# Optimization experiments

Hardware: AMD Instinct MI355X
Metric: run time of the kernel (lower is better)

## Reference

```python
import jax, jax.numpy as jnp
import numpy as np

LR = 0.01  # constraint relaxation learning rate (module default)
EPS = 1e-6


def setup_inputs() -> dict:
    key = jax.random.key(0)
    k1, k2, k3, k4 = jax.random.split(key, 4)
    N, E, K = 8192, 262144, 65536
    positions = jax.random.normal(k1, (N, 3), dtype=jnp.float32)
    edge_index = jax.random.randint(k2, (2, E), 0, N, dtype=jnp.int32)
    dist_idx = jax.random.randint(k3, (K, 2), 0, N, dtype=jnp.int32)
    dist_target = jax.random.uniform(k4, (K,), dtype=jnp.float32) * 2.0
    min_dist = jnp.ones((1,), dtype=jnp.float32) * 0.5
    return {"positions": positions, "edge_index": edge_index,
            "dist_idx": dist_idx, "dist_target": dist_target,
            "min_dist": min_dist}


def reference(positions, edge_index, dist_idx, dist_target, min_dist):
    x = positions  # (N, 3)
    N = x.shape[0]

    # --- distance constraints: ||x_i - x_j|| -> d_ij (Jacobi-style update) ---
    i, j = dist_idx[:, 0], dist_idx[:, 1]
    vec = x[i] - x[j]                                  # (K, 3)
    dist = jnp.sqrt(jnp.sum(vec * vec, axis=-1) + 1e-12)
    valid = (dist > EPS) & (i != j)
    coef = jnp.where(valid, LR * 0.5 * (dist - dist_target) / dist, 0.0)
    corr = coef[:, None] * vec                         # (K, 3)
    x = x.at[i].add(-corr).at[j].add(corr)

    # --- collision constraints: push apart all pairs with dist < min_dist ---
    md = min_dist[0]
    sq = jnp.sum(x * x, axis=-1)                       # (N,)
    d2 = jnp.maximum(sq[:, None] + sq[None, :] - 2.0 * (x @ x.T), 1e-12)
    dmat = jnp.sqrt(d2)                                # (N, N) pairwise distances
    mask = (dmat < md) & (dmat > EPS)                  # excludes diagonal (dist ~ 0)
    w = jnp.where(mask, (md - dmat) / dmat, 0.0) * (0.5 * LR)  # (N, N)
    # correction_i = sum_j w_ij * (x_i - x_j)
    x = x + x * jnp.sum(w, axis=-1, keepdims=True) - w @ x

    # --- gaussian curvature via normalized graph Laplacian ---
    e = jnp.clip(edge_index, 0, N - 1)
    adj = jnp.zeros((N, N), dtype=x.dtype).at[e[0], e[1]].set(1.0)
    adj = adj + adj.T
    deg = adj.sum(axis=1)
    dinv = jnp.where(deg == 0, 0.0, jnp.power(deg + EPS, -0.5))
    # L_norm @ x = x - D^{-1/2} A D^{-1/2} x (diagonal scaling, same math)
    lap = x - dinv[:, None] * (adj @ (dinv[:, None] * x))
    curvature = jnp.sqrt(jnp.sum(lap * lap, axis=-1) + 1e-12)  # (N,)

    return x, curvature
```

## Files before the change

### kernel.cpp

```cpp
#include <hip/hip_runtime.h>
#include <math.h>

#define N_NODES 8192
#define WPR 256
#define LR_C 0.01f
#define EPS_C 1e-6f
#define NJ 32

__global__ __launch_bounds__(256) void init_clear(const float4* __restrict__ pos4,
                                                  float4* __restrict__ x1_4,
                                                  uint4* __restrict__ adj,
                                                  uint4* __restrict__ deg4) {
    int gid = blockIdx.x * blockDim.x + threadIdx.x;
    adj[gid] = make_uint4(0u, 0u, 0u, 0u);
    if (gid < 6144) x1_4[gid] = pos4[gid];
    if (gid < 2048) deg4[gid] = make_uint4(0u, 0u, 0u, 0u);
}

__global__ __launch_bounds__(256) void scatter_adj(
        const float* __restrict__ x0, const int* __restrict__ dist_idx,
        const float* __restrict__ dist_target, const int* __restrict__ edge_index,
        float* __restrict__ x1, unsigned int* __restrict__ A,
        unsigned int* __restrict__ B, int* __restrict__ deg,
        int K, int E, int nbK) {
    int blk = blockIdx.x;
    if (blk < nbK) {
        int k = blk * 256 + threadIdx.x;
        if (k >= K) return;
        int i = dist_idx[2 * k], j = dist_idx[2 * k + 1];
        float ax = x0[3 * i], ay = x0[3 * i + 1], az = x0[3 * i + 2];
        float bx = x0[3 * j], by = x0[3 * j + 1], bz = x0[3 * j + 2];
        float vx = ax - bx, vy = ay - by, vz = az - bz;
        float dist = sqrtf(vx * vx + vy * vy + vz * vz + 1e-12f);
        bool valid = (dist > EPS_C) && (i != j);
        float coef = valid ? (LR_C * 0.5f) * (dist - dist_target[k]) / dist : 0.0f;
        if (coef != 0.0f) {
            float cx = coef * vx, cy = coef * vy, cz = coef * vz;
            atomicAdd(&x1[3 * i],     -cx);
            atomicAdd(&x1[3 * i + 1], -cy);
            atomicAdd(&x1[3 * i + 2], -cz);
            atomicAdd(&x1[3 * j],      cx);
            atomicAdd(&x1[3 * j + 1],  cy);
            atomicAdd(&x1[3 * j + 2],  cz);
        }
    } else {
        int k = (blk - nbK) * 256 + threadIdx.x;
        if (k >= E) return;
        int a = edge_index[k];
        int b = edge_index[E + k];
        a = min(max(a, 0), N_NODES - 1);
        b = min(max(b, 0), N_NODES - 1);
        unsigned int bitb = 1u << (b & 31);
        unsigned int bita = 1u << (a & 31);
        unsigned int old = atomicOr(&A[a * WPR + (b >> 5)], bitb);
        if (!(old & bitb)) atomicAdd(&deg[a], 1);
        old = atomicOr(&B[b * WPR + (a >> 5)], bita);
        if (!(old & bita)) atomicAdd(&deg[b], 1);
    }
}

__global__ __launch_bounds__(256) void repulsion_partial(
        const float* __restrict__ x1, const float* __restrict__ min_dist,
        float4* __restrict__ partials) {
    __shared__ float4 pj[256];
    int t = threadIdx.x;
    int jbase = blockIdx.y * 256;
    int i = blockIdx.x * 256 + t;
    {
        int j = jbase + t;
        float a = x1[3 * j], b = x1[3 * j + 1], c = x1[3 * j + 2];
        pj[t] = make_float4(a, b, c, a * a + b * b + c * c);
    }
    __syncthreads();
    float xi = x1[3 * i], yi = x1[3 * i + 1], zi = x1[3 * i + 2];
    float sqi = xi * xi + yi * yi + zi * zi;
    float md = min_dist[0];
    const float c0 = 0.5f * LR_C;
    float c1 = c0 * md;
    float S = 0.f, axc = 0.f, ayc = 0.f, azc = 0.f;
    if (blockIdx.x == blockIdx.y) {
        int di = t;
        #pragma unroll 4
        for (int jj = 0; jj < 256; ++jj) {
            float4 p = pj[jj];
            float dot = fmaf(xi, p.x, fmaf(yi, p.y, zi * p.z));
            float d2 = fmaf(-2.0f, dot, sqi + p.w);
            float r = __builtin_amdgcn_rsqf(fmaxf(d2, 1e-12f));
            float w = fmaxf(fmaf(c1, r, -c0), 0.0f);
            w = (d2 > 1e-12f && jj != di) ? w : 0.0f;
            S += w;
            axc = fmaf(w, p.x, axc);
            ayc = fmaf(w, p.y, ayc);
            azc = fmaf(w, p.z, azc);
        }
    } else {
        #pragma unroll 4
        for (int jj = 0; jj < 256; ++jj) {
            float4 p = pj[jj];
            float dot = fmaf(xi, p.x, fmaf(yi, p.y, zi * p.z));
            float d2 = fmaf(-2.0f, dot, sqi + p.w);
            float r = __builtin_amdgcn_rsqf(fmaxf(d2, 1e-12f));
            float w = fmaxf(fmaf(c1, r, -c0), 0.0f);
            w = (d2 > 1e-12f) ? w : 0.0f;
            S += w;
            axc = fmaf(w, p.x, axc);
            ayc = fmaf(w, p.y, ayc);
            azc = fmaf(w, p.z, azc);
        }
    }
    partials[blockIdx.y * N_NODES + i] = make_float4(axc, ayc, azc, S);
}

__global__ __launch_bounds__(256) void finalize(
        const float* __restrict__ x1, const float4* __restrict__ partials,
        const int* __restrict__ deg,
        float* __restrict__ x2, float* __restrict__ out_x,
        float* __restrict__ dinv, float4* __restrict__ z4) {
    int i = blockIdx.x * blockDim.x + threadIdx.x;
    if (i >= N_NODES) return;
    float S = 0.f, axc = 0.f, ayc = 0.f, azc = 0.f;
    #pragma unroll
    for (int c = 0; c < NJ; ++c) {
        float4 p = partials[c * N_NODES + i];
        axc += p.x; ayc += p.y; azc += p.z; S += p.w;
    }
    float xi = x1[3 * i], yi = x1[3 * i + 1], zi = x1[3 * i + 2];
    float ox = xi + xi * S - axc;
    float oy = yi + yi * S - ayc;
    float oz = zi + zi * S - azc;
    x2[3 * i] = ox; x2[3 * i + 1] = oy; x2[3 * i + 2] = oz;
    out_x[3 * i] = ox; out_x[3 * i + 1] = oy; out_x[3 * i + 2] = oz;
    int d = deg[i];
    float dv = (d == 0) ? 0.0f : 1.0f / sqrtf((float)d + EPS_C);
    dinv[i] = dv;
    z4[i] = make_float4(dv * ox, dv * oy, dv * oz, dv);
}

__global__ __launch_bounds__(256) void lap_kernel(
        const unsigned int* __restrict__ A, const unsigned int* __restrict__ B,
        const float* __restrict__ x2, const float* __restrict__ dinv,
        const float4* __restrict__ z4, float* __restrict__ out_curv) {
    int row = (blockIdx.x * blockDim.x + threadIdx.x) >> 6;
    int lane = threadIdx.x & 63;
    if (row >= N_NODES) return;
    float axc = 0.f, ayc = 0.f, azc = 0.f;
    #pragma unroll
    for (int q = 0; q < 4; ++q) {
        int wi = q * 64 + lane;
        unsigned int w = A[(size_t)row * WPR + wi];
        while (w) {
            int b = __ffs(w) - 1; w &= w - 1;
            float4 z = z4[wi * 32 + b];
            axc += z.x; ayc += z.y; azc += z.z;
        }
        w = B[(size_t)row * WPR + wi];
        while (w) {
            int b = __ffs(w) - 1; w &= w - 1;
            float4 z = z4[wi * 32 + b];
            axc += z.x; ayc += z.y; azc += z.z;
        }
    }
    for (int off = 32; off; off >>= 1) {
        axc += __shfl_down(axc, off);
        ayc += __shfl_down(ayc, off);
        azc += __shfl_down(azc, off);
    }
    if (lane == 0) {
        float dv = dinv[row];
        float lx = x2[3 * row]     - dv * axc;
        float ly = x2[3 * row + 1] - dv * ayc;
        float lz = x2[3 * row + 2] - dv * azc;
        out_curv[row] = sqrtf(lx * lx + ly * ly + lz * lz + 1e-12f);
    }
}

extern "C" void kernel_launch(void* const* d_in, const int* in_sizes, int n_in,
                              void* d_out, int out_size, void* d_ws, size_t ws_size,
                              hipStream_t stream) {
    const float* positions   = (const float*)d_in[0];
    const int*   edge_index  = (const int*)d_in[1];
    const int*   dist_idx    = (const int*)d_in[2];
    const float* dist_target = (const float*)d_in[3];
    const float* min_dist    = (const float*)d_in[4];
    float* out = (float*)d_out;

    const int E = in_sizes[1] / 2;
    const int K = in_sizes[2] / 2;

    char* ws = (char*)d_ws;
    const size_t X1_OFF   = 0;
    const size_t X2_OFF   = X1_OFF + (size_t)N_NODES * 3 * 4;
    const size_t Z4_OFF   = X2_OFF + (size_t)N_NODES * 3 * 4;
    const size_t DINV_OFF = Z4_OFF + (size_t)N_NODES * 16;
    const size_t DEG_OFF  = DINV_OFF + (size_t)N_NODES * 4;
    const size_t PART_OFF = DEG_OFF + (size_t)N_NODES * 4;
    const size_t ADJ_OFF  = PART_OFF + (size_t)NJ * N_NODES * 16;
    const size_t ADJ_BYTES = (size_t)N_NODES * WPR * 4;

    float* x1         = (float*)(ws + X1_OFF);
    float* x2         = (float*)(ws + X2_OFF);
    float4* z4        = (float4*)(ws + Z4_OFF);
    float* dinv       = (float*)(ws + DINV_OFF);
    int*   deg        = (int*)(ws + DEG_OFF);
    float4* partials  = (float4*)(ws + PART_OFF);
    unsigned int* A   = (unsigned int*)(ws + ADJ_OFF);
    unsigned int* B   = (unsigned int*)(ws + ADJ_OFF + ADJ_BYTES);

    init_clear<<<4096, 256, 0, stream>>>((const float4*)positions,
                                         (float4*)x1, (uint4*)A, (uint4*)deg);

    int nbK = (K + 255) / 256;
    int nbE = (E + 255) / 256;
    scatter_adj<<<nbK + nbE, 256, 0, stream>>>(
        positions, dist_idx, dist_target, edge_index, x1, A, B, deg, K, E, nbK);

    dim3 grid_rep(N_NODES / 256, NJ);
    repulsion_partial<<<grid_rep, 256, 0, stream>>>(x1, min_dist, partials);

    finalize<<<N_NODES / 256, 256, 0, stream>>>(x1, partials, deg,
                                                x2, out, dinv, z4);

    lap_kernel<<<N_NODES / 4, 256, 0, stream>>>(A, B, x2, dinv, z4,
                                                out + 3 * N_NODES);
}
```

Measured before the change: 118.5 us.

## Replace dense adjacency bitmaps with hashed edge dedup and atomic Laplacian scatter

Drops the two dense N×N adjacency bitmaps, which cost 16 MB to clear and a full row scan in the Laplacian kernel. Edges are now deduplicated with an open-addressing hash on (a,b) keys via atomicCAS, and each edge gets a uniqueness flag. The Laplacian becomes a per-edge atomic scatter of z4 into an accumulator, followed by a small curvature kernel. In exchange it adds hash probing contention, float atomics (nondeterministic summation order) and one extra kernel launch.

```diff
diff --git a/kernel.cpp b/kernel.cpp
--- a/kernel.cpp
+++ b/kernel.cpp
@@ -2,26 +2,43 @@
 #include <math.h>
 
 #define N_NODES 8192
-#define WPR 256
 #define LR_C 0.01f
 #define EPS_C 1e-6f
 #define NJ 32
+#define HASH_SLOTS (1u << 20)
+#define HEMPTY 0xFFFFFFFFu
+
+#define HASH_V 262144
+#define X1_V   6144
+#define LACC_V 6144
+#define DEG_V  2048
+#define TOT_V  (HASH_V + X1_V + LACC_V + DEG_V)
 
 __global__ __launch_bounds__(256) void init_clear(const float4* __restrict__ pos4,
                                                   float4* __restrict__ x1_4,
-                                                  uint4* __restrict__ adj,
+                                                  uint4* __restrict__ hash4,
+                                                  float4* __restrict__ lacc4,
                                                   uint4* __restrict__ deg4) {
     int gid = blockIdx.x * blockDim.x + threadIdx.x;
-    adj[gid] = make_uint4(0u, 0u, 0u, 0u);
-    if (gid < 6144) x1_4[gid] = pos4[gid];
-    if (gid < 2048) deg4[gid] = make_uint4(0u, 0u, 0u, 0u);
-}
-
-__global__ __launch_bounds__(256) void scatter_adj(
+    if (gid < HASH_V) {
+        hash4[gid] = make_uint4(HEMPTY, HEMPTY, HEMPTY, HEMPTY);
+    } else if (gid < HASH_V + X1_V) {
+        int t = gid - HASH_V;
+        x1_4[t] = pos4[t];
+    } else if (gid < HASH_V + X1_V + LACC_V) {
+        int t = gid - (HASH_V + X1_V);
+        lacc4[t] = make_float4(0.f, 0.f, 0.f, 0.f);
+    } else if (gid < TOT_V) {
+        int t = gid - (HASH_V + X1_V + LACC_V);
+        deg4[t] = make_uint4(0u, 0u, 0u, 0u);
+    }
+}
+
+__global__ __launch_bounds__(256) void scatter_hash(
         const float* __restrict__ x0, const int* __restrict__ dist_idx,
         const float* __restrict__ dist_target, const int* __restrict__ edge_index,
-        float* __restrict__ x1, unsigned int* __restrict__ A,
-        unsigned int* __restrict__ B, int* __restrict__ deg,
+        float* __restrict__ x1, unsigned int* __restrict__ hash,
+        unsigned char* __restrict__ flags, int* __restrict__ deg,
         int K, int E, int nbK) {
     int blk = blockIdx.x;
     if (blk < nbK) {
@@ -50,12 +67,20 @@
         int b = edge_index[E + k];
         a = min(max(a, 0), N_NODES - 1);
         b = min(max(b, 0), N_NODES - 1);
-        unsigned int bitb = 1u << (b & 31);
-        unsigned int bita = 1u << (a & 31);
-        unsigned int old = atomicOr(&A[a * WPR + (b >> 5)], bitb);
-        if (!(old & bitb)) atomicAdd(&deg[a], 1);
-        old = atomicOr(&B[b * WPR + (a >> 5)], bita);
-        if (!(old & bita)) atomicAdd(&deg[b], 1);
+        unsigned int key = ((unsigned)a << 13) | (unsigned)b;
+        unsigned int h = (key * 2654435761u) >> 12;
+        bool unique = false;
+        while (true) {
+            unsigned int old = atomicCAS(&hash[h], HEMPTY, key);
+            if (old == HEMPTY) { unique = true; break; }
+            if (old == key)   { break; }
+            h = (h + 1) & (HASH_SLOTS - 1);
+        }
+        flags[k] = unique ? 1 : 0;
+        if (unique) {
+            atomicAdd(&deg[a], 1);
+            atomicAdd(&deg[b], 1);
+        }
     }
 }
 
@@ -136,42 +161,36 @@
     z4[i] = make_float4(dv * ox, dv * oy, dv * oz, dv);
 }
 
-__global__ __launch_bounds__(256) void lap_kernel(
-        const unsigned int* __restrict__ A, const unsigned int* __restrict__ B,
+__global__ __launch_bounds__(256) void lap_scatter(
+        const int* __restrict__ edge_index, const unsigned char* __restrict__ flags,
+        const float4* __restrict__ z4, float* __restrict__ lacc, int E) {
+    int k = blockIdx.x * blockDim.x + threadIdx.x;
+    if (k >= E) return;
+    if (!flags[k]) return;
+    int a = edge_index[k];
+    int b = edge_index[E + k];
+    a = min(max(a, 0), N_NODES - 1);
+    b = min(max(b, 0), N_NODES - 1);
+    float4 zb = z4[b];
+    float4 za = z4[a];
+    atomicAdd(&lacc[3 * a],     zb.x);
+    atomicAdd(&lacc[3 * a + 1], zb.y);
+    atomicAdd(&lacc[3 * a + 2], zb.z);
+    atomicAdd(&lacc[3 * b],     za.x);
+    atomicAdd(&lacc[3 * b + 1], za.y);
+    atomicAdd(&lacc[3 * b + 2], za.z);
+}
+
+__global__ __launch_bounds__(256) void curvature(
         const float* __restrict__ x2, const float* __restrict__ dinv,
-        const float4* __restrict__ z4, float* __restrict__ out_curv) {
-    int row = (blockIdx.x * blockDim.x + threadIdx.x) >> 6;
-    int lane = threadIdx.x & 63;
-    if (row >= N_NODES) return;
-    float axc = 0.f, ayc = 0.f, azc = 0.f;
-    #pragma unroll
-    for (int q = 0; q < 4; ++q) {
-        int wi = q * 64 + lane;
-        unsigned int w = A[(size_t)row * WPR + wi];
-        while (w) {
-            int b = __ffs(w) - 1; w &= w - 1;
-            float4 z = z4[wi * 32 + b];
-            axc += z.x; ayc += z.y; azc += z.z;
-        }
-        w = B[(size_t)row * WPR + wi];
-        while (w) {
-            int b = __ffs(w) - 1; w &= w - 1;
-            float4 z = z4[wi * 32 + b];
-            axc += z.x; ayc += z.y; azc += z.z;
-        }
-    }
-    for (int off = 32; off; off >>= 1) {
-        axc += __shfl_down(axc, off);
-        ayc += __shfl_down(ayc, off);
-        azc += __shfl_down(azc, off);
-    }
-    if (lane == 0) {
-        float dv = dinv[row];
-        float lx = x2[3 * row]     - dv * axc;
-        float ly = x2[3 * row + 1] - dv * ayc;
-        float lz = x2[3 * row + 2] - dv * azc;
-        out_curv[row] = sqrtf(lx * lx + ly * ly + lz * lz + 1e-12f);
-    }
+        const float* __restrict__ lacc, float* __restrict__ out_curv) {
+    int i = blockIdx.x * blockDim.x + threadIdx.x;
+    if (i >= N_NODES) return;
+    float dv = dinv[i];
+    float lx = x2[3 * i]     - dv * lacc[3 * i];
+    float ly = x2[3 * i + 1] - dv * lacc[3 * i + 1];
+    float lz = x2[3 * i + 2] - dv * lacc[3 * i + 2];
+    out_curv[i] = sqrtf(lx * lx + ly * ly + lz * lz + 1e-12f);
 }
 
 extern "C" void kernel_launch(void* const* d_in, const int* in_sizes, int n_in,
@@ -193,26 +212,30 @@
     const size_t Z4_OFF   = X2_OFF + (size_t)N_NODES * 3 * 4;
     const size_t DINV_OFF = Z4_OFF + (size_t)N_NODES * 16;
     const size_t DEG_OFF  = DINV_OFF + (size_t)N_NODES * 4;
-    const size_t PART_OFF = DEG_OFF + (size_t)N_NODES * 4;
-    const size_t ADJ_OFF  = PART_OFF + (size_t)NJ * N_NODES * 16;
-    const size_t ADJ_BYTES = (size_t)N_NODES * WPR * 4;
-
-    float* x1         = (float*)(ws + X1_OFF);
-    float* x2         = (float*)(ws + X2_OFF);
-    float4* z4        = (float4*)(ws + Z4_OFF);
-    float* dinv       = (float*)(ws + DINV_OFF);
-    int*   deg        = (int*)(ws + DEG_OFF);
-    float4* partials  = (float4*)(ws + PART_OFF);
-    unsigned int* A   = (unsigned int*)(ws + ADJ_OFF);
-    unsigned int* B   = (unsigned int*)(ws + ADJ_OFF + ADJ_BYTES);
-
-    init_clear<<<4096, 256, 0, stream>>>((const float4*)positions,
-                                         (float4*)x1, (uint4*)A, (uint4*)deg);
+    const size_t LACC_OFF = DEG_OFF + (size_t)N_NODES * 4;
+    const size_t FLAG_OFF = LACC_OFF + (size_t)N_NODES * 3 * 4;
+    const size_t PART_OFF = FLAG_OFF + (size_t)E;
+    const size_t HASH_OFF = PART_OFF + (size_t)NJ * N_NODES * 16;
+
+    float* x1            = (float*)(ws + X1_OFF);
+    float* x2            = (float*)(ws + X2_OFF);
+    float4* z4           = (float4*)(ws + Z4_OFF);
+    float* dinv          = (float*)(ws + DINV_OFF);
+    int*   deg           = (int*)(ws + DEG_OFF);
+    float* lacc          = (float*)(ws + LACC_OFF);
+    unsigned char* flags = (unsigned char*)(ws + FLAG_OFF);
+    float4* partials     = (float4*)(ws + PART_OFF);
+    unsigned int* hash   = (unsigned int*)(ws + HASH_OFF);
+
+    init_clear<<<TOT_V / 256, 256, 0, stream>>>(
+        (const float4*)positions, (float4*)x1, (uint4*)hash,
+        (float4*)lacc, (uint4*)deg);
 
     int nbK = (K + 255) / 256;
     int nbE = (E + 255) / 256;
-    scatter_adj<<<nbK + nbE, 256, 0, stream>>>(
-        positions, dist_idx, dist_target, edge_index, x1, A, B, deg, K, E, nbK);
+    scatter_hash<<<nbK + nbE, 256, 0, stream>>>(
+        positions, dist_idx, dist_target, edge_index,
+        x1, hash, flags, deg, K, E, nbK);
 
     dim3 grid_rep(N_NODES / 256, NJ);
     repulsion_partial<<<grid_rep, 256, 0, stream>>>(x1, min_dist, partials);
@@ -220,6 +243,8 @@
     finalize<<<N_NODES / 256, 256, 0, stream>>>(x1, partials, deg,
                                                 x2, out, dinv, z4);
 
-    lap_kernel<<<N_NODES / 4, 256, 0, stream>>>(A, B, x2, dinv, z4,
-                                                out + 3 * N_NODES);
-}
+    lap_scatter<<<nbE, 256, 0, stream>>>(edge_index, flags, z4, lacc, E);
+
+    curvature<<<N_NODES / 256, 256, 0, stream>>>(x2, dinv, lacc,
+                                                 out + 3 * N_NODES);
+}
```

New measurement: 175.1 us. +47.8%, slower.
